# Performance work log

Hardware: AMD Instinct MI355X
Metric: run time of the kernel (lower is better)

The kernel has to match this reference:

```python
import jax, jax.numpy as jnp
import numpy as np

B, C, N, D = 4, 128, 4096, 128  # batch, channels (=d_tran=out), points
BN_EPS = 1e-5


def setup_inputs() -> dict:
    key = jax.random.key(0)
    ks = jax.random.split(key, 10)
    s = 1.0 / np.sqrt(C)
    return {
        "x": jax.random.normal(ks[0], (B, C, N), dtype=jnp.float32),
        "Wqk": jax.random.uniform(ks[1], (D, C), minval=-s, maxval=s, dtype=jnp.float32),  # shared q/k weight
        "Wv": jax.random.uniform(ks[2], (D, C), minval=-s, maxval=s, dtype=jnp.float32),
        "bv": jax.random.uniform(ks[3], (D,), minval=-s, maxval=s, dtype=jnp.float32),
        "Wt": jax.random.uniform(ks[4], (C, D), minval=-s, maxval=s, dtype=jnp.float32),
        "bt": jax.random.uniform(ks[5], (C,), minval=-s, maxval=s, dtype=jnp.float32),
        "gamma": jnp.ones((C,), dtype=jnp.float32) + 0.1 * jax.random.normal(ks[6], (C,), dtype=jnp.float32),
        "beta": 0.1 * jax.random.normal(ks[7], (C,), dtype=jnp.float32),
        "rmean": 0.1 * jax.random.normal(ks[8], (C,), dtype=jnp.float32),
        "rvar": jax.random.uniform(ks[9], (C,), minval=0.5, maxval=1.5, dtype=jnp.float32),
    }


def reference(x, Wqk, Wv, bv, Wt, bt, gamma, beta, rmean, rvar):
    # x: [B, C, N]; 1x1 convs are per-point matmuls over the channel dim.
    x_q = jnp.einsum('dc,bcn->bnd', Wqk, x)                 # [B, N, D]
    x_k = jnp.einsum('dc,bcn->bdn', Wqk, x)                 # [B, D, N] (tied weight)
    x_v = jnp.einsum('dc,bcn->bdn', Wv, x) + bv[None, :, None]
    energy = jnp.einsum('bnd,bdm->bnm', x_q, x_k)           # [B, N, N]
    attention = jax.nn.softmax(energy, axis=-1)             # row softmax
    attention = attention / (1e-9 + attention.sum(axis=1, keepdims=True))  # L1 over columns
    x_r = jnp.einsum('bdn,bnm->bdm', x_v, attention)        # [B, D, N]
    y = jnp.einsum('od,bdn->bon', Wt, x - x_r) + bt[None, :, None]
    # BatchNorm1d, inference mode (running stats)
    y = gamma[None, :, None] * (y - rmean[None, :, None]) * jax.lax.rsqrt(rvar[None, :, None] + BN_EPS) + beta[None, :, None]
    return x + jax.nn.relu(y)
```

## Files before the change

### kernel.cpp

```cpp
#include <hip/hip_runtime.h>
#include <hip/hip_bf16.h>

typedef unsigned int u32;
typedef unsigned short u16;
using bf16x8 = __attribute__((ext_vector_type(8))) short;
using f32x4  = __attribute__((ext_vector_type(4))) float;
using f32x16 = __attribute__((ext_vector_type(16))) float;

#define B_ 4
#define C_ 128
#define N_ 4096
#define D_ 128
#define NS1 8
#define NSEG (N_ / NS1)
#define NCH (NSEG / 32)
#define NS2 6
#define NCHUNK (N_ / 32)

#define QS_STRIDE 136
#define VS_STRIDE 40

__device__ __forceinline__ u16 f2bf(float f) {
    u32 x = __builtin_bit_cast(u32, f);
    x = x + 0x7fffu + ((x >> 16) & 1u);
    return (u16)(x >> 16);
}
__device__ __forceinline__ float bf2f(u16 h) {
    return __builtin_bit_cast(float, (u32)h << 16);
}
__device__ __forceinline__ u32 cvtpk(float lo, float hi) {
    u32 d;
    asm("v_cvt_pk_bf16_f32 %0, %1, %2" : "=v"(d) : "v"(lo), "v"(hi));
    return d;
}
#define EXP2 __builtin_amdgcn_exp2f
__device__ __forceinline__ bf16x8 pack8(const float* v, float s) {
    bf16x8 r;
#pragma unroll
    for (int j = 0; j < 8; ++j) r[j] = (short)f2bf(v[j] * s);
    return r;
}

__global__ __launch_bounds__(256) void k_proj(
        const float* __restrict__ x, const float* __restrict__ Wqk,
        const float* __restrict__ Wv, const float* __restrict__ bv,
        u16* __restrict__ Qbf, u16* __restrict__ Vbf) {
    __shared__ float xs[C_ * 65];
    const int bid = blockIdx.x;
    const int b  = bid >> 6;
    const int n0 = (bid & 63) << 6;
    const int t  = threadIdx.x;
    const float* xb = x + (size_t)b * C_ * N_;
    for (int i = 0; i < 32; ++i) {
        int idx = i * 256 + t;
        int c = idx >> 6, n = idx & 63;
        xs[c * 65 + n] = xb[(size_t)c * N_ + n0 + n];
    }
    __syncthreads();
    const int lane = t & 63, w = t >> 6;
    const int l15 = lane & 15, g = lane >> 4;
    const float SC = 1.2011224087864498f;

    bf16x8 xf[4];
#pragma unroll
    for (int kk = 0; kk < 4; ++kk) {
        float tmp[8];
#pragma unroll
        for (int j = 0; j < 8; ++j) tmp[j] = xs[(kk * 32 + g * 8 + j) * 65 + (16 * w + l15)];
        xf[kk] = pack8(tmp, 1.0f);
    }
    for (int dt = 0; dt < 8; ++dt) {
        const int d = dt * 16 + l15;
        bf16x8 wq[4], wv[4];
#pragma unroll
        for (int kk = 0; kk < 4; ++kk) {
            const float* pq = Wqk + (size_t)d * C_ + kk * 32 + g * 8;
            const float* pv = Wv  + (size_t)d * C_ + kk * 32 + g * 8;
            float a[8], c8[8];
#pragma unroll
            for (int j = 0; j < 8; ++j) { a[j] = pq[j]; c8[j] = pv[j]; }
            wq[kk] = pack8(a, SC);
            wv[kk] = pack8(c8, 1.0f);
        }
        f32x4 aq = {0.f, 0.f, 0.f, 0.f}, av = {0.f, 0.f, 0.f, 0.f};
#pragma unroll
        for (int kk = 0; kk < 4; ++kk) {
            aq = __builtin_amdgcn_mfma_f32_16x16x32_bf16(xf[kk], wq[kk], aq, 0, 0, 0);
            av = __builtin_amdgcn_mfma_f32_16x16x32_bf16(wv[kk], xf[kk], av, 0, 0, 0);
        }
#pragma unroll
        for (int r = 0; r < 4; ++r) {
            int nn = n0 + 16 * w + g * 4 + r;
            Qbf[((size_t)b * N_ + nn) * D_ + dt * 16 + l15] = f2bf(aq[r]);
            int dd = dt * 16 + g * 4 + r;
            Vbf[((size_t)b * D_ + dd) * N_ + n0 + 16 * w + l15] = f2bf(av[r] + bv[dd]);
        }
    }
}

__global__ __launch_bounds__(256, 4) void k_pass1(const u16* __restrict__ Qbf,
                                                  float* __restrict__ rsp) {
    __shared__ __align__(16) u16 qs[2][32 * QS_STRIDE];
    int bid = blockIdx.x;
    const int s = bid & 7; bid >>= 3;
    const int ntile = bid & 31; const int b = bid >> 5;
    const int t = threadIdx.x, lane = t & 63, w = t >> 6;
    const int l31 = lane & 31, hi = lane >> 5;
    const int nb = ntile * 128 + w * 32;

    bf16x8 bqn[8];
    {
        const u16* qn = Qbf + ((size_t)b * N_ + nb + l31) * D_ + hi * 8;
#pragma unroll
        for (int dblk = 0; dblk < 8; ++dblk) bqn[dblk] = *(const bf16x8*)(qn + dblk * 16);
    }
    const int srow = t >> 4, sslot = t & 15;
    const u16* qsrc = Qbf + ((size_t)b * N_ + s * NSEG + srow) * D_ + sslot * 8;
    const int qoff = srow * QS_STRIDE + sslot * 8;

    {
        uint4 a0 = *(const uint4*)qsrc;
        uint4 a1 = *(const uint4*)(qsrc + (size_t)16 * D_);
        *(uint4*)&qs[0][qoff] = a0;
        *(uint4*)&qs[0][qoff + 16 * QS_STRIDE] = a1;
    }
    __syncthreads();

    float rs0 = 0.f, rs1 = 0.f;
    for (int mc = 0; mc < NCH; ++mc) {
        const int cur = mc & 1;
        uint4 qpre0, qpre1;
        if (mc < NCH - 1) {
            qpre0 = *(const uint4*)(qsrc + (size_t)(mc + 1) * 32 * D_);
            qpre1 = *(const uint4*)(qsrc + (size_t)((mc + 1) * 32 + 16) * D_);
        }
        f32x16 ea, eb;
#pragma unroll
        for (int i = 0; i < 16; ++i) { ea[i] = 0.f; eb[i] = 0.f; }
#pragma unroll
        for (int dblk = 0; dblk < 4; ++dblk) {
            bf16x8 am0 = *(const bf16x8*)(qs[cur] + l31 * QS_STRIDE + (2 * dblk + hi) * 8);
            bf16x8 am1 = *(const bf16x8*)(qs[cur] + l31 * QS_STRIDE + (2 * (dblk + 4) + hi) * 8);
            ea = __builtin_amdgcn_mfma_f32_32x32x16_bf16(am0, bqn[dblk], ea, 0, 0, 0);
            eb = __builtin_amdgcn_mfma_f32_32x32x16_bf16(am1, bqn[dblk + 4], eb, 0, 0, 0);
        }
#pragma unroll
        for (int r = 0; r < 16; r += 2) {
            rs0 += EXP2(ea[r] + eb[r] - 64.0f);
            rs1 += EXP2(ea[r + 1] + eb[r + 1] - 64.0f);
        }
        if (mc < NCH - 1) {
            *(uint4*)&qs[cur ^ 1][qoff] = qpre0;
            *(uint4*)&qs[cur ^ 1][qoff + 16 * QS_STRIDE] = qpre1;
        }
        __syncthreads();
    }
    float rs = rs0 + rs1;
    rs += __shfl_xor(rs, 32);
    if (lane < 32) rsp[((size_t)s * B_ + b) * N_ + nb + l31] = rs;
}

__global__ void k_irs(const float* __restrict__ rsp, float* __restrict__ irs) {
    int i = blockIdx.x * 256 + threadIdx.x;
    if (i < B_ * N_) {
        float s = 0.f;
#pragma unroll
        for (int sp = 0; sp < NS1; ++sp) s += rsp[(size_t)sp * B_ * N_ + i];
        irs[i] = 1.0f / s;
    }
}

__global__ __launch_bounds__(256, 3) void k_pass2(
        const u16* __restrict__ Qbf, const u16* __restrict__ Vbf,
        const float* __restrict__ irs, u32* __restrict__ Rp32,
        float* __restrict__ csp) {
    __shared__ __align__(16) u16 qs[2][32 * QS_STRIDE];
    __shared__ __align__(16) u16 vs[2][128 * VS_STRIDE];
    int bid = blockIdx.x;
    const int s = bid % NS2; bid /= NS2;
    const int mtile = bid & 31; const int b = bid >> 5;
    const int t = threadIdx.x, lane = t & 63, w = t >> 6;
    const int l31 = lane & 31, hi = lane >> 5;
    const int m0 = mtile * 128 + w * 32;

    bf16x8 bq[8];
    {
        const u16* qm = Qbf + ((size_t)b * N_ + m0 + l31) * D_ + hi * 8;
#pragma unroll
        for (int dblk = 0; dblk < 8; ++dblk) bq[dblk] = *(const bf16x8*)(qm + dblk * 16);
    }
    f32x16 acc[4];
#pragma unroll
    for (int i = 0; i < 4; ++i)
#pragma unroll
        for (int r = 0; r < 16; ++r) acc[i][r] = 0.f;
    float cs = 0.f;
    const float* irsb = irs + (size_t)b * N_;

    const int qrow = t >> 4, qslot = t & 15;
    const u16* qsrc = Qbf + ((size_t)b * N_ + qrow) * D_ + qslot * 8;
    const int qoff = qrow * QS_STRIDE + qslot * 8;
    const int vd = t >> 2, vslot = t & 3;
    const u16* vsrc = Vbf + ((size_t)b * D_ + vd) * N_ + vslot * 8;
    const int voff = vd * VS_STRIDE + vslot * 8;

    {
        const u16* q0 = qsrc + (size_t)s * 32 * D_;
        const u16* v0 = vsrc + s * 32;
        uint4 a0 = *(const uint4*)q0;
        uint4 a1 = *(const uint4*)(q0 + (size_t)16 * D_);
        uint4 b0 = *(const uint4*)v0;
        uint4 b1 = *(const uint4*)(v0 + (size_t)64 * N_);
        *(uint4*)&qs[0][qoff] = a0;
        *(uint4*)&qs[0][qoff + 16 * QS_STRIDE] = a1;
        *(uint4*)&vs[0][voff] = b0;
        *(uint4*)&vs[0][voff + 64 * VS_STRIDE] = b1;
    }
    __syncthreads();

    int iter = 0;
    for (int c = s; c < NCHUNK; c += NS2, ++iter) {
        const int cur = iter & 1;
        const int nb = c * 32;
        const int cn = c + NS2;
        uint4 qpre0, qpre1, vpre0, vpre1;
        if (cn < NCHUNK) {
            const u16* qn = qsrc + (size_t)cn * 32 * D_;
            const u16* vn = vsrc + cn * 32;
            qpre0 = *(const uint4*)qn;
            qpre1 = *(const uint4*)(qn + (size_t)16 * D_);
            vpre0 = *(const uint4*)vn;
            vpre1 = *(const uint4*)(vn + (size_t)64 * N_);
        }
        const float* irp = irsb + nb;
        float si[32];
#pragma unroll
        for (int j = 0; j < 32; ++j) si[j] = irp[j];

        f32x16 ea, eb;
#pragma unroll
        for (int i = 0; i < 16; ++i) { ea[i] = 0.f; eb[i] = 0.f; }
#pragma unroll
        for (int dblk = 0; dblk < 4; ++dblk) {
            bf16x8 aq0 = *(const bf16x8*)(qs[cur] + l31 * QS_STRIDE + (2 * dblk + hi) * 8);
            bf16x8 aq1 = *(const bf16x8*)(qs[cur] + l31 * QS_STRIDE + (2 * (dblk + 4) + hi) * 8);
            ea = __builtin_amdgcn_mfma_f32_32x32x16_bf16(aq0, bq[dblk], ea, 0, 0, 0);
            eb = __builtin_amdgcn_mfma_f32_32x32x16_bf16(aq1, bq[dblk + 4], eb, 0, 0, 0);
        }
        uint4 bpA0, bpA1;
        {
            u32 A[8];
#pragma unroll
            for (int i = 0; i < 8; ++i) {
                const int cc = 2 * (i & 1) + 8 * (i >> 1);
                float ir0 = hi ? si[cc + 4] : si[cc];
                float ir1 = hi ? si[cc + 5] : si[cc + 1];
                float p0 = EXP2(ea[2 * i] + eb[2 * i] - 64.0f) * ir0;
                float p1 = EXP2(ea[2 * i + 1] + eb[2 * i + 1] - 64.0f) * ir1;
                cs += p0 + p1;
                A[i] = cvtpk(p0, p1);
            }
            u32 X0 = (u32)__shfl_xor((int)A[0], 32), X1 = (u32)__shfl_xor((int)A[1], 32);
            u32 X2 = (u32)__shfl_xor((int)A[2], 32), X3 = (u32)__shfl_xor((int)A[3], 32);
            u32 X4 = (u32)__shfl_xor((int)A[4], 32), X5 = (u32)__shfl_xor((int)A[5], 32);
            u32 X6 = (u32)__shfl_xor((int)A[6], 32), X7 = (u32)__shfl_xor((int)A[7], 32);
            bpA0 = (uint4){hi ? X2 : A[0], hi ? X3 : A[1], hi ? A[2] : X0, hi ? A[3] : X1};
            bpA1 = (uint4){hi ? X6 : A[4], hi ? X7 : A[5], hi ? A[6] : X4, hi ? A[7] : X5};
        }
#pragma unroll
        for (int nblk = 0; nblk < 2; ++nblk) {
            bf16x8 bp = __builtin_bit_cast(bf16x8, nblk ? bpA1 : bpA0);
#pragma unroll
            for (int dblk = 0; dblk < 4; ++dblk) {
                bf16x8 av = *(const bf16x8*)(vs[cur] + (dblk * 32 + l31) * VS_STRIDE +
                                             (nblk * 2 + hi) * 8);
                acc[dblk] = __builtin_amdgcn_mfma_f32_32x32x16_bf16(av, bp, acc[dblk], 0, 0, 0);
            }
        }
        if (cn < NCHUNK) {
            *(uint4*)&qs[cur ^ 1][qoff] = qpre0;
            *(uint4*)&qs[cur ^ 1][qoff + 16 * QS_STRIDE] = qpre1;
            *(uint4*)&vs[cur ^ 1][voff] = vpre0;
            *(uint4*)&vs[cur ^ 1][voff + 64 * VS_STRIDE] = vpre1;
        }
        __syncthreads();
    }
    cs += __shfl_xor(cs, 32);
    if (lane < 32) csp[((size_t)s * B_ + b) * N_ + m0 + l31] = cs;
    u32* rpb = Rp32 + ((size_t)s * B_ + b) * (size_t)(D_ / 2) * N_;
#pragma unroll
    for (int dblk = 0; dblk < 4; ++dblk) {
#pragma unroll
        for (int j = 0; j < 8; ++j) {
            const int row = dblk * 16 + (j & 1) + 4 * (j >> 1) + 2 * hi;
            u32 pk = cvtpk(acc[dblk][2 * j], acc[dblk][2 * j + 1]);
            rpb[(size_t)row * N_ + m0 + l31] = pk;
        }
    }
}

__global__ __launch_bounds__(512) void k_final(
        const float* __restrict__ x, const float* __restrict__ Wt,
        const float* __restrict__ bt, const float* __restrict__ gamma,
        const float* __restrict__ beta, const float* __restrict__ rmean,
        const float* __restrict__ rvar, const u32* __restrict__ Rp32,
        const float* __restrict__ csp, float* __restrict__ out) {
    __shared__ float us[128 * 65];
    __shared__ float icss[64];
    const int bid = blockIdx.x;
    const int b = bid >> 6;
    const int n0 = (bid & 63) << 6;
    const int t = threadIdx.x, lane = t & 63, w = t >> 6;
    const int l15 = lane & 15, g = lane >> 4;
    if (t < 64) {
        float s = 0.f;
#pragma unroll
        for (int sp = 0; sp < NS2; ++sp)
            s += csp[((size_t)sp * B_ + b) * N_ + n0 + t];
        icss[t] = 1.0f / (1e-9f + s);
    }
    __syncthreads();
    const float* xb = x + (size_t)b * C_ * N_;
    for (int i = 0; i < 8; ++i) {
        int idx = i * 512 + t;
        int dp = idx >> 6, n = idx & 63;
        float r0 = 0.f, r1 = 0.f;
#pragma unroll
        for (int sp = 0; sp < NS2; ++sp) {
            u32 v = Rp32[(((size_t)(sp * B_ + b) * (D_ / 2)) + dp) * N_ + n0 + n];
            r0 += bf2f((u16)(v & 0xffffu));
            r1 += bf2f((u16)(v >> 16));
        }
        float ic = icss[n];
        us[(2 * dp) * 65 + n]     = xb[(size_t)(2 * dp) * N_ + n0 + n]     - r0 * ic;
        us[(2 * dp + 1) * 65 + n] = xb[(size_t)(2 * dp + 1) * N_ + n0 + n] - r1 * ic;
    }
    __syncthreads();
    const int cg = w & 3;
    const int ct0 = (w >> 2) * 4;
    bf16x8 uf[4];
#pragma unroll
    for (int kk = 0; kk < 4; ++kk) {
        float tmp[8];
#pragma unroll
        for (int j = 0; j < 8; ++j) tmp[j] = us[(kk * 32 + g * 8 + j) * 65 + (16 * cg + l15)];
        uf[kk] = pack8(tmp, 1.0f);
    }
    for (int cti = 0; cti < 4; ++cti) {
        const int ct = ct0 + cti;
        const int c = ct * 16 + l15;
        bf16x8 wf[4];
#pragma unroll
        for (int kk = 0; kk < 4; ++kk) {
            const float* p = Wt + (size_t)c * D_ + kk * 32 + g * 8;
            float a[8];
#pragma unroll
            for (int j = 0; j < 8; ++j) a[j] = p[j];
            wf[kk] = pack8(a, 1.0f);
        }
        f32x4 acc = {0.f, 0.f, 0.f, 0.f};
#pragma unroll
        for (int kk = 0; kk < 4; ++kk)
            acc = __builtin_amdgcn_mfma_f32_16x16x32_bf16(wf[kk], uf[kk], acc, 0, 0, 0);
#pragma unroll
        for (int r = 0; r < 4; ++r) {
            const int cc = ct * 16 + g * 4 + r;
            const int nn = n0 + 16 * cg + l15;
            float y = acc[r] + bt[cc];
            float bn = gamma[cc] * (y - rmean[cc]) * rsqrtf(rvar[cc] + 1e-5f) + beta[cc];
            float rl = fmaxf(bn, 0.0f);
            out[((size_t)b * C_ + cc) * N_ + nn] = xb[(size_t)cc * N_ + nn] + rl;
        }
    }
}

extern "C" void kernel_launch(void* const* d_in, const int* in_sizes, int n_in,
                              void* d_out, int out_size, void* d_ws, size_t ws_size,
                              hipStream_t stream) {
    (void)in_sizes; (void)n_in; (void)out_size; (void)ws_size;
    const float* x     = (const float*)d_in[0];
    const float* Wqk   = (const float*)d_in[1];
    const float* Wv    = (const float*)d_in[2];
    const float* bv    = (const float*)d_in[3];
    const float* Wt    = (const float*)d_in[4];
    const float* bt    = (const float*)d_in[5];
    const float* gamma = (const float*)d_in[6];
    const float* beta  = (const float*)d_in[7];
    const float* rmean = (const float*)d_in[8];
    const float* rvar  = (const float*)d_in[9];
    float* out = (float*)d_out;

    char* ws = (char*)d_ws;
    u16*   Qbf = (u16*)(ws);
    u16*   Vbf = (u16*)(ws + 4194304);
    float* rsp = (float*)(ws + 8388608);
    float* irs = (float*)(ws + 8912896);
    float* csp = (float*)(ws + 8978432);
    u32*   Rp  = (u32*)(ws + 9371648);

    k_proj  <<<B_ * 64,       256, 0, stream>>>(x, Wqk, Wv, bv, Qbf, Vbf);
    k_pass1 <<<B_ * 32 * NS1, 256, 0, stream>>>(Qbf, rsp);
    k_irs   <<<(B_ * N_ + 255) / 256, 256, 0, stream>>>(rsp, irs);
    k_pass2 <<<B_ * 32 * NS2, 256, 0, stream>>>(Qbf, Vbf, irs, Rp, csp);
    k_final <<<B_ * 64,       512, 0, stream>>>(x, Wt, bt, gamma, beta, rmean, rvar, Rp, csp, out);
}
```

Before: 117.3 us.

## Stage Q/V tiles via direct global-to-LDS loads with XOR swizzle

```diff
diff --git a/kernel.cpp b/kernel.cpp
--- a/kernel.cpp
+++ b/kernel.cpp
@@ -11,14 +11,9 @@
 #define C_ 128
 #define N_ 4096
 #define D_ 128
-#define NS1 8
-#define NSEG (N_ / NS1)
-#define NCH (NSEG / 32)
+#define NS1 10
 #define NS2 6
 #define NCHUNK (N_ / 32)
-
-#define QS_STRIDE 136
-#define VS_STRIDE 40
 
 __device__ __forceinline__ u16 f2bf(float f) {
     u32 x = __builtin_bit_cast(u32, f);
@@ -34,6 +29,11 @@
     return d;
 }
 #define EXP2 __builtin_amdgcn_exp2f
+__device__ __forceinline__ void gload16(const u16* g, u16* l) {
+    __builtin_amdgcn_global_load_lds(
+        (const __attribute__((address_space(1))) u32*)g,
+        (__attribute__((address_space(3))) u32*)l, 16, 0, 0);
+}
 __device__ __forceinline__ bf16x8 pack8(const float* v, float s) {
     bf16x8 r;
 #pragma unroll
@@ -98,11 +98,11 @@
     }
 }
 
-__global__ __launch_bounds__(256, 4) void k_pass1(const u16* __restrict__ Qbf,
+__global__ __launch_bounds__(256, 5) void k_pass1(const u16* __restrict__ Qbf,
                                                   float* __restrict__ rsp) {
-    __shared__ __align__(16) u16 qs[2][32 * QS_STRIDE];
+    __shared__ __align__(16) u16 qs[2][32 * 128];
     int bid = blockIdx.x;
-    const int s = bid & 7; bid >>= 3;
+    const int s = bid % NS1; bid /= NS1;
     const int ntile = bid & 31; const int b = bid >> 5;
     const int t = threadIdx.x, lane = t & 63, w = t >> 6;
     const int l31 = lane & 31, hi = lane >> 5;
@@ -114,33 +114,30 @@
 #pragma unroll
         for (int dblk = 0; dblk < 8; ++dblk) bqn[dblk] = *(const bf16x8*)(qn + dblk * 16);
     }
-    const int srow = t >> 4, sslot = t & 15;
-    const u16* qsrc = Qbf + ((size_t)b * N_ + s * NSEG + srow) * D_ + sslot * 8;
-    const int qoff = srow * QS_STRIDE + sslot * 8;
-
-    {
-        uint4 a0 = *(const uint4*)qsrc;
-        uint4 a1 = *(const uint4*)(qsrc + (size_t)16 * D_);
-        *(uint4*)&qs[0][qoff] = a0;
-        *(uint4*)&qs[0][qoff + 16 * QS_STRIDE] = a1;
-    }
+    const int qrow = t >> 4, qslot = t & 15;
+    const u16* qsrc = Qbf + ((size_t)b * N_ + qrow) * D_ + ((qslot ^ (qrow & 7)) * 8);
+    const int swq = (l31 & 7);
+
+    gload16(qsrc + (size_t)s * 32 * D_, &qs[0][w * 512]);
+    gload16(qsrc + (size_t)(s * 32 + 16) * D_, &qs[0][2048 + w * 512]);
     __syncthreads();
 
     float rs0 = 0.f, rs1 = 0.f;
-    for (int mc = 0; mc < NCH; ++mc) {
-        const int cur = mc & 1;
-        uint4 qpre0, qpre1;
-        if (mc < NCH - 1) {
-            qpre0 = *(const uint4*)(qsrc + (size_t)(mc + 1) * 32 * D_);
-            qpre1 = *(const uint4*)(qsrc + (size_t)((mc + 1) * 32 + 16) * D_);
+    int iter = 0;
+    for (int c = s; c < NCHUNK; c += NS1, ++iter) {
+        const int cur = iter & 1;
+        const int cn = c + NS1;
+        if (cn < NCHUNK) {
+            gload16(qsrc + (size_t)cn * 32 * D_, &qs[cur ^ 1][w * 512]);
+            gload16(qsrc + (size_t)(cn * 32 + 16) * D_, &qs[cur ^ 1][2048 + w * 512]);
         }
         f32x16 ea, eb;
 #pragma unroll
         for (int i = 0; i < 16; ++i) { ea[i] = 0.f; eb[i] = 0.f; }
 #pragma unroll
         for (int dblk = 0; dblk < 4; ++dblk) {
-            bf16x8 am0 = *(const bf16x8*)(qs[cur] + l31 * QS_STRIDE + (2 * dblk + hi) * 8);
-            bf16x8 am1 = *(const bf16x8*)(qs[cur] + l31 * QS_STRIDE + (2 * (dblk + 4) + hi) * 8);
+            bf16x8 am0 = *(const bf16x8*)&qs[cur][l31 * 128 + (((2 * dblk + hi) ^ swq) * 8)];
+            bf16x8 am1 = *(const bf16x8*)&qs[cur][l31 * 128 + (((2 * (dblk + 4) + hi) ^ swq) * 8)];
             ea = __builtin_amdgcn_mfma_f32_32x32x16_bf16(am0, bqn[dblk], ea, 0, 0, 0);
             eb = __builtin_amdgcn_mfma_f32_32x32x16_bf16(am1, bqn[dblk + 4], eb, 0, 0, 0);
         }
@@ -148,10 +145,6 @@
         for (int r = 0; r < 16; r += 2) {
             rs0 += EXP2(ea[r] + eb[r] - 64.0f);
             rs1 += EXP2(ea[r + 1] + eb[r + 1] - 64.0f);
-        }
-        if (mc < NCH - 1) {
-            *(uint4*)&qs[cur ^ 1][qoff] = qpre0;
-            *(uint4*)&qs[cur ^ 1][qoff + 16 * QS_STRIDE] = qpre1;
         }
         __syncthreads();
     }
@@ -174,8 +167,8 @@
         const u16* __restrict__ Qbf, const u16* __restrict__ Vbf,
         const float* __restrict__ irs, u32* __restrict__ Rp32,
         float* __restrict__ csp) {
-    __shared__ __align__(16) u16 qs[2][32 * QS_STRIDE];
-    __shared__ __align__(16) u16 vs[2][128 * VS_STRIDE];
+    __shared__ __align__(16) u16 qs[2][32 * 128];
+    __shared__ __align__(16) u16 vs[2][128 * 32];
     int bid = blockIdx.x;
     const int s = bid % NS2; bid /= NS2;
     const int mtile = bid & 31; const int b = bid >> 5;
@@ -198,24 +191,17 @@
     const float* irsb = irs + (size_t)b * N_;
 
     const int qrow = t >> 4, qslot = t & 15;
-    const u16* qsrc = Qbf + ((size_t)b * N_ + qrow) * D_ + qslot * 8;
-    const int qoff = qrow * QS_STRIDE + qslot * 8;
+    const u16* qsrc = Qbf + ((size_t)b * N_ + qrow) * D_ + ((qslot ^ (qrow & 7)) * 8);
     const int vd = t >> 2, vslot = t & 3;
-    const u16* vsrc = Vbf + ((size_t)b * D_ + vd) * N_ + vslot * 8;
-    const int voff = vd * VS_STRIDE + vslot * 8;
-
-    {
-        const u16* q0 = qsrc + (size_t)s * 32 * D_;
-        const u16* v0 = vsrc + s * 32;
-        uint4 a0 = *(const uint4*)q0;
-        uint4 a1 = *(const uint4*)(q0 + (size_t)16 * D_);
-        uint4 b0 = *(const uint4*)v0;
-        uint4 b1 = *(const uint4*)(v0 + (size_t)64 * N_);
-        *(uint4*)&qs[0][qoff] = a0;
-        *(uint4*)&qs[0][qoff + 16 * QS_STRIDE] = a1;
-        *(uint4*)&vs[0][voff] = b0;
-        *(uint4*)&vs[0][voff + 64 * VS_STRIDE] = b1;
-    }
+    const u16* vsrc0 = Vbf + ((size_t)b * D_ + vd) * N_ + ((vslot ^ ((vd >> 1) & 3)) * 8);
+    const u16* vsrc1 = vsrc0 + (size_t)64 * N_;
+    const int swq = (l31 & 7);
+    const int swv = ((l31 >> 1) & 3);
+
+    gload16(qsrc + (size_t)s * 32 * D_, &qs[0][w * 512]);
+    gload16(qsrc + (size_t)(s * 32 + 16) * D_, &qs[0][2048 + w * 512]);
+    gload16(vsrc0 + s * 32, &vs[0][w * 512]);
+    gload16(vsrc1 + s * 32, &vs[0][2048 + w * 512]);
     __syncthreads();
 
     int iter = 0;
@@ -223,14 +209,11 @@
         const int cur = iter & 1;
         const int nb = c * 32;
         const int cn = c + NS2;
-        uint4 qpre0, qpre1, vpre0, vpre1;
         if (cn < NCHUNK) {
-            const u16* qn = qsrc + (size_t)cn * 32 * D_;
-            const u16* vn = vsrc + cn * 32;
-            qpre0 = *(const uint4*)qn;
-            qpre1 = *(const uint4*)(qn + (size_t)16 * D_);
-            vpre0 = *(const uint4*)vn;
-            vpre1 = *(const uint4*)(vn + (size_t)64 * N_);
+            gload16(qsrc + (size_t)cn * 32 * D_, &qs[cur ^ 1][w * 512]);
+            gload16(qsrc + (size_t)(cn * 32 + 16) * D_, &qs[cur ^ 1][2048 + w * 512]);
+            gload16(vsrc0 + cn * 32, &vs[cur ^ 1][w * 512]);
+            gload16(vsrc1 + cn * 32, &vs[cur ^ 1][2048 + w * 512]);
         }
         const float* irp = irsb + nb;
         float si[32];
@@ -242,8 +225,8 @@
         for (int i = 0; i < 16; ++i) { ea[i] = 0.f; eb[i] = 0.f; }
 #pragma unroll
         for (int dblk = 0; dblk < 4; ++dblk) {
-            bf16x8 aq0 = *(const bf16x8*)(qs[cur] + l31 * QS_STRIDE + (2 * dblk + hi) * 8);
-            bf16x8 aq1 = *(const bf16x8*)(qs[cur] + l31 * QS_STRIDE + (2 * (dblk + 4) + hi) * 8);
+            bf16x8 aq0 = *(const bf16x8*)&qs[cur][l31 * 128 + (((2 * dblk + hi) ^ swq) * 8)];
+            bf16x8 aq1 = *(const bf16x8*)&qs[cur][l31 * 128 + (((2 * (dblk + 4) + hi) ^ swq) * 8)];
             ea = __builtin_amdgcn_mfma_f32_32x32x16_bf16(aq0, bq[dblk], ea, 0, 0, 0);
             eb = __builtin_amdgcn_mfma_f32_32x32x16_bf16(aq1, bq[dblk + 4], eb, 0, 0, 0);
         }
@@ -272,16 +255,10 @@
             bf16x8 bp = __builtin_bit_cast(bf16x8, nblk ? bpA1 : bpA0);
 #pragma unroll
             for (int dblk = 0; dblk < 4; ++dblk) {
-                bf16x8 av = *(const bf16x8*)(vs[cur] + (dblk * 32 + l31) * VS_STRIDE +
-                                             (nblk * 2 + hi) * 8);
+                bf16x8 av = *(const bf16x8*)&vs[cur][(dblk * 32 + l31) * 32 +
+                                                    (((nblk * 2 + hi) ^ swv) * 8)];
                 acc[dblk] = __builtin_amdgcn_mfma_f32_32x32x16_bf16(av, bp, acc[dblk], 0, 0, 0);
             }
-        }
-        if (cn < NCHUNK) {
-            *(uint4*)&qs[cur ^ 1][qoff] = qpre0;
-            *(uint4*)&qs[cur ^ 1][qoff + 16 * QS_STRIDE] = qpre1;
-            *(uint4*)&vs[cur ^ 1][voff] = vpre0;
-            *(uint4*)&vs[cur ^ 1][voff + 64 * VS_STRIDE] = vpre1;
         }
         __syncthreads();
     }
@@ -394,9 +371,9 @@
     u16*   Qbf = (u16*)(ws);
     u16*   Vbf = (u16*)(ws + 4194304);
     float* rsp = (float*)(ws + 8388608);
-    float* irs = (float*)(ws + 8912896);
-    float* csp = (float*)(ws + 8978432);
-    u32*   Rp  = (u32*)(ws + 9371648);
+    float* irs = (float*)(ws + 9043968);
+    float* csp = (float*)(ws + 9109504);
+    u32*   Rp  = (u32*)(ws + 9502720);
 
     k_proj  <<<B_ * 64,       256, 0, stream>>>(x, Wqk, Wv, bv, Qbf, Vbf);
     k_pass1 <<<B_ * 32 * NS1, 256, 0, stream>>>(Qbf, rsp);
```

New measurement: 118.7 us. Within noise of the previous version (+1.1%).
